# Optimization experiments

Hardware: AMD Instinct MI355X
Metric: run time of the kernel (lower is better)

The kernel has to match this reference:

```python
import jax, jax.numpy as jnp
import numpy as np

B, T, H = 64, 4096, 512


def setup_inputs() -> dict:
    key = jax.random.key(0)
    ks = jax.random.split(key, 6)
    x = jax.random.normal(ks[0], (B, T), dtype=jnp.float32)
    # a ~ U(0.95, 0.999) as in torch init (stable decay)
    a = jax.random.uniform(ks[1], (H,), dtype=jnp.float32, minval=0.95, maxval=0.999)
    b = jax.random.uniform(ks[2], (H,), dtype=jnp.float32, minval=-0.5, maxval=0.5)
    c = jax.random.uniform(ks[3], (H,), dtype=jnp.float32, minval=-0.1, maxval=0.1)
    w = jax.random.uniform(ks[4], (H,), dtype=jnp.float32, minval=-0.5, maxval=0.5)
    e = jax.random.uniform(ks[5], (1,), dtype=jnp.float32, minval=-0.1, maxval=0.1)
    return {"x": x, "a": a, "b": b, "c": c, "w": w, "e": e}


def reference(x, a, b, c, w, e):
    # x: [B, T]; a, b, c, w: [H]; e: [1]
    batch = x.shape[0]
    hidden = a.shape[0]

    def step(h, x_t):
        # h: [B, H]; x_t: [B]
        h = a * h + b * x_t[:, None] + c
        return h, None

    h0 = jnp.zeros((batch, hidden), dtype=x.dtype)
    h, _ = jax.lax.scan(step, h0, x.T)  # scan over T
    z = h @ w + e  # [B]
    return z
```

## Files before the change

### kernel.cpp

```cpp
#include <hip/hip_runtime.h>

#define T_LEN 4096
#define H_LEN 512
#define B_LEN 64

__global__ void build_g_kernel(const float* __restrict__ a,
                               const float* __restrict__ b,
                               const float* __restrict__ c,
                               const float* __restrict__ w,
                               const float* __restrict__ e,
                               float* __restrict__ g,
                               float* __restrict__ Kc)
{
    const int tid = threadIdx.x;
    if (blockIdx.x < T_LEN / 64) {
        __shared__ float wb[H_LEN];
        __shared__ float l2a[H_LEN];
        for (int j = tid; j < H_LEN; j += 256) {
            wb[j]  = w[j] * b[j];
            l2a[j] = log2f(a[j]);
        }
        __syncthreads();
        const int   tt = tid & 63;
        const int   jq = tid >> 6;
        const int   t  = blockIdx.x * 64 + tt;
        const float k  = (float)(T_LEN - 1 - t);
        const int   j0 = jq * (H_LEN / 4);
        float s = 0.f;
#pragma unroll 8
        for (int jj = 0; jj < H_LEN / 4; ++jj) {
            const int j = j0 + jj;
            s += wb[j] * exp2f(k * l2a[j]);
        }
        __shared__ float part[4][64];
        part[jq][tt] = s;
        __syncthreads();
        if (tid < 64) {
            g[blockIdx.x * 64 + tid] =
                part[0][tid] + part[1][tid] + part[2][tid] + part[3][tid];
        }
    } else {
        __shared__ double red[256];
        double s = 0.0;
        for (int j = tid; j < H_LEN; j += 256) {
            const double aj  = (double)a[j];
            const double geo = (1.0 - pow(aj, (double)T_LEN)) / (1.0 - aj);
            s += (double)w[j] * (double)c[j] * geo;
        }
        red[tid] = s;
        __syncthreads();
        for (int off = 128; off > 0; off >>= 1) {
            if (tid < off) red[tid] += red[tid + off];
            __syncthreads();
        }
        if (tid == 0) Kc[0] = (float)(red[0] + (double)e[0]);
    }
}

__global__ void dot_kernel(const float* __restrict__ x,
                           const float* __restrict__ g,
                           const float* __restrict__ Kc,
                           float* __restrict__ z)
{
    const int row = blockIdx.x;
    const int tid = threadIdx.x;
    const float4* __restrict__ xr = (const float4*)(x + (size_t)row * T_LEN);
    const float4* __restrict__ gv = (const float4*)g;
    float s = 0.f;
#pragma unroll
    for (int i = tid; i < T_LEN / 4; i += 256) {
        const float4 xv = xr[i];
        const float4 gg = gv[i];
        s += xv.x * gg.x + xv.y * gg.y + xv.z * gg.z + xv.w * gg.w;
    }
#pragma unroll
    for (int off = 32; off > 0; off >>= 1)
        s += __shfl_down(s, off, 64);
    __shared__ float wsum[4];
    const int wave = tid >> 6;
    if ((tid & 63) == 0) wsum[wave] = s;
    __syncthreads();
    if (tid == 0) {
        z[row] = wsum[0] + wsum[1] + wsum[2] + wsum[3] + Kc[0];
    }
}

extern "C" void kernel_launch(void* const* d_in, const int* in_sizes, int n_in,
                              void* d_out, int out_size, void* d_ws, size_t ws_size,
                              hipStream_t stream) {
    const float* x = (const float*)d_in[0];
    const float* a = (const float*)d_in[1];
    const float* b = (const float*)d_in[2];
    const float* c = (const float*)d_in[3];
    const float* w = (const float*)d_in[4];
    const float* e = (const float*)d_in[5];
    float* out = (float*)d_out;

    float* g  = (float*)d_ws;
    float* Kc = g + T_LEN;

    build_g_kernel<<<T_LEN / 64 + 1, 256, 0, stream>>>(a, b, c, w, e, g, Kc);
    dot_kernel<<<B_LEN, 256, 0, stream>>>(x, g, Kc, out);
}
```

Measured before the change: 68.21 us.

## Fuse weight-kernel build and dot product into one kernel with grid barrier

Merges the two launches into a single kernel. The 64 g-building blocks each also own one batch row of x: they preload it, compute their slice of g, then meet at an atomic counter barrier, waiting on a flag set by the extra Kc block, before doing the dot product. This removes the second launch and the gap between the two kernels, and overlaps the x loads with the exp2 work. In exchange it relies on all blocks being co-resident. The flag is never reset, so on repeated calls a block could increment the counter before the Kc block resets it, which risks a hang.

```diff
diff --git a/kernel.cpp b/kernel.cpp
--- a/kernel.cpp
+++ b/kernel.cpp
@@ -3,43 +3,27 @@
 #define T_LEN 4096
 #define H_LEN 512
 #define B_LEN 64
+#define NGBLK (T_LEN / 64)
 
-__global__ void build_g_kernel(const float* __restrict__ a,
-                               const float* __restrict__ b,
-                               const float* __restrict__ c,
-                               const float* __restrict__ w,
-                               const float* __restrict__ e,
-                               float* __restrict__ g,
-                               float* __restrict__ Kc)
+__global__ __launch_bounds__(256) void fused_kernel(
+    const float* __restrict__ x,
+    const float* __restrict__ a,
+    const float* __restrict__ b,
+    const float* __restrict__ c,
+    const float* __restrict__ w,
+    const float* __restrict__ e,
+    float* __restrict__ g,
+    float* __restrict__ Kc,
+    unsigned int* __restrict__ C,
+    unsigned int* __restrict__ F,
+    float* __restrict__ z)
 {
     const int tid = threadIdx.x;
-    if (blockIdx.x < T_LEN / 64) {
-        __shared__ float wb[H_LEN];
-        __shared__ float l2a[H_LEN];
-        for (int j = tid; j < H_LEN; j += 256) {
-            wb[j]  = w[j] * b[j];
-            l2a[j] = log2f(a[j]);
-        }
-        __syncthreads();
-        const int   tt = tid & 63;
-        const int   jq = tid >> 6;
-        const int   t  = blockIdx.x * 64 + tt;
-        const float k  = (float)(T_LEN - 1 - t);
-        const int   j0 = jq * (H_LEN / 4);
-        float s = 0.f;
-#pragma unroll 8
-        for (int jj = 0; jj < H_LEN / 4; ++jj) {
-            const int j = j0 + jj;
-            s += wb[j] * exp2f(k * l2a[j]);
-        }
-        __shared__ float part[4][64];
-        part[jq][tt] = s;
-        __syncthreads();
-        if (tid < 64) {
-            g[blockIdx.x * 64 + tid] =
-                part[0][tid] + part[1][tid] + part[2][tid] + part[3][tid];
-        }
-    } else {
+    const int blk = blockIdx.x;
+
+    if (blk == NGBLK) {
+        if (tid == 0)
+            __hip_atomic_store(C, 0u, __ATOMIC_RELEASE, __HIP_MEMORY_SCOPE_AGENT);
         __shared__ double red[256];
         double s = 0.0;
         for (int j = tid; j < H_LEN; j += 256) {
@@ -53,36 +37,71 @@
             if (tid < off) red[tid] += red[tid + off];
             __syncthreads();
         }
-        if (tid == 0) Kc[0] = (float)(red[0] + (double)e[0]);
+        if (tid == 0) {
+            Kc[0] = (float)(red[0] + (double)e[0]);
+            __threadfence();
+            __hip_atomic_store(F, 1u, __ATOMIC_RELEASE, __HIP_MEMORY_SCOPE_AGENT);
+        }
+        return;
     }
-}
 
-__global__ void dot_kernel(const float* __restrict__ x,
-                           const float* __restrict__ g,
-                           const float* __restrict__ Kc,
-                           float* __restrict__ z)
-{
-    const int row = blockIdx.x;
-    const int tid = threadIdx.x;
-    const float4* __restrict__ xr = (const float4*)(x + (size_t)row * T_LEN);
+    const float4* __restrict__ xr = (const float4*)(x + (size_t)blk * T_LEN);
+    const float4 xv0 = xr[tid];
+    const float4 xv1 = xr[tid + 256];
+    const float4 xv2 = xr[tid + 512];
+    const float4 xv3 = xr[tid + 768];
+
+    __shared__ float wb[H_LEN];
+    __shared__ float l2a[H_LEN];
+    for (int j = tid; j < H_LEN; j += 256) {
+        wb[j]  = w[j] * b[j];
+        l2a[j] = log2f(a[j]);
+    }
+    __syncthreads();
+    const int   tt = tid & 63;
+    const int   jq = tid >> 6;
+    const int   t  = blk * 64 + tt;
+    const float k  = (float)(T_LEN - 1 - t);
+    const int   j0 = jq * (H_LEN / 4);
+    float s = 0.f;
+#pragma unroll 8
+    for (int jj = 0; jj < H_LEN / 4; ++jj) {
+        const int j = j0 + jj;
+        s += wb[j] * exp2f(k * l2a[j]);
+    }
+    __shared__ float part[4][64];
+    part[jq][tt] = s;
+    __syncthreads();
+    if (tid < 64)
+        g[blk * 64 + tid] = part[0][tid] + part[1][tid] + part[2][tid] + part[3][tid];
+
+    __syncthreads();
+    if (tid == 0) {
+        __threadfence();
+        while (__hip_atomic_load(F, __ATOMIC_ACQUIRE, __HIP_MEMORY_SCOPE_AGENT) != 1u) {}
+        __hip_atomic_fetch_add(C, 1u, __ATOMIC_ACQ_REL, __HIP_MEMORY_SCOPE_AGENT);
+        while (__hip_atomic_load(C, __ATOMIC_ACQUIRE, __HIP_MEMORY_SCOPE_AGENT) != (unsigned)NGBLK) {}
+    }
+    __syncthreads();
+    __threadfence();
+
     const float4* __restrict__ gv = (const float4*)g;
-    float s = 0.f;
-#pragma unroll
-    for (int i = tid; i < T_LEN / 4; i += 256) {
-        const float4 xv = xr[i];
-        const float4 gg = gv[i];
-        s += xv.x * gg.x + xv.y * gg.y + xv.z * gg.z + xv.w * gg.w;
-    }
+    const float4 g0 = gv[tid];
+    const float4 g1 = gv[tid + 256];
+    const float4 g2 = gv[tid + 512];
+    const float4 g3 = gv[tid + 768];
+    float d = xv0.x * g0.x + xv0.y * g0.y + xv0.z * g0.z + xv0.w * g0.w
+            + xv1.x * g1.x + xv1.y * g1.y + xv1.z * g1.z + xv1.w * g1.w
+            + xv2.x * g2.x + xv2.y * g2.y + xv2.z * g2.z + xv2.w * g2.w
+            + xv3.x * g3.x + xv3.y * g3.y + xv3.z * g3.z + xv3.w * g3.w;
 #pragma unroll
     for (int off = 32; off > 0; off >>= 1)
-        s += __shfl_down(s, off, 64);
+        d += __shfl_down(d, off, 64);
     __shared__ float wsum[4];
-    const int wave = tid >> 6;
-    if ((tid & 63) == 0) wsum[wave] = s;
+    if ((tid & 63) == 0) wsum[tid >> 6] = d;
     __syncthreads();
-    if (tid == 0) {
-        z[row] = wsum[0] + wsum[1] + wsum[2] + wsum[3] + Kc[0];
-    }
+    if (tid == 0)
+        z[blk] = wsum[0] + wsum[1] + wsum[2] + wsum[3] + Kc[0];
 }
 
 extern "C" void kernel_launch(void* const* d_in, const int* in_sizes, int n_in,
@@ -96,9 +115,10 @@
     const float* e = (const float*)d_in[5];
     float* out = (float*)d_out;
 
-    float* g  = (float*)d_ws;
-    float* Kc = g + T_LEN;
+    float*        g  = (float*)d_ws;
+    float*        Kc = g + T_LEN;
+    unsigned int* C  = (unsigned int*)(Kc + 1);
+    unsigned int* F  = C + 1;
 
-    build_g_kernel<<<T_LEN / 64 + 1, 256, 0, stream>>>(a, b, c, w, e, g, Kc);
-    dot_kernel<<<B_LEN, 256, 0, stream>>>(x, g, Kc, out);
+    fused_kernel<<<NGBLK + 1, 256, 0, stream>>>(x, a, b, c, w, e, g, Kc, C, F, out);
 }
```

Measured after the change: 74.71 us. 9.5% more time.

## Fuse g-vector construction with per-chunk dot products, reduce partials in finish kernel

Applied to the files above, without the earlier changes.

Each of the 64 time-chunk blocks now builds its slice of the decay-weighted vector g in shared memory and immediately dots it against the matching 64-column slice of x for all 64 rows. It writes per-row, per-chunk partial sums. A single-block finish kernel computes the constant bias term and sums the partials per row. This removes the global round trip for g and spreads the x read across 64 blocks instead of one block per row. The cost is an extra partials buffer and a serial single-block finish stage that also carries the double-precision geometric-sum work.

```diff
diff --git a/kernel.cpp b/kernel.cpp
--- a/kernel.cpp
+++ b/kernel.cpp
@@ -3,85 +3,94 @@
 #define T_LEN 4096
 #define H_LEN 512
 #define B_LEN 64
+#define NCHUNK (T_LEN / 64)
 
-__global__ void build_g_kernel(const float* __restrict__ a,
-                               const float* __restrict__ b,
-                               const float* __restrict__ c,
-                               const float* __restrict__ w,
-                               const float* __restrict__ e,
-                               float* __restrict__ g,
-                               float* __restrict__ Kc)
+__global__ __launch_bounds__(256) void chunk_kernel(
+    const float* __restrict__ x,
+    const float* __restrict__ a,
+    const float* __restrict__ b,
+    const float* __restrict__ w,
+    float* __restrict__ partials)
 {
     const int tid = threadIdx.x;
-    if (blockIdx.x < T_LEN / 64) {
-        __shared__ float wb[H_LEN];
-        __shared__ float l2a[H_LEN];
-        for (int j = tid; j < H_LEN; j += 256) {
-            wb[j]  = w[j] * b[j];
-            l2a[j] = log2f(a[j]);
-        }
-        __syncthreads();
-        const int   tt = tid & 63;
-        const int   jq = tid >> 6;
-        const int   t  = blockIdx.x * 64 + tt;
-        const float k  = (float)(T_LEN - 1 - t);
-        const int   j0 = jq * (H_LEN / 4);
-        float s = 0.f;
+    const int blk = blockIdx.x;
+
+    __shared__ float wb[H_LEN];
+    __shared__ float l2a[H_LEN];
+    for (int j = tid; j < H_LEN; j += 256) {
+        wb[j]  = w[j] * b[j];
+        l2a[j] = log2f(a[j]);
+    }
+    __syncthreads();
+    const int   tt = tid & 63;
+    const int   jq = tid >> 6;
+    const float k  = (float)(T_LEN - 1 - (blk * 64 + tt));
+    const int   j0 = jq * (H_LEN / 4);
+    float s = 0.f;
 #pragma unroll 8
-        for (int jj = 0; jj < H_LEN / 4; ++jj) {
-            const int j = j0 + jj;
-            s += wb[j] * exp2f(k * l2a[j]);
-        }
-        __shared__ float part[4][64];
-        part[jq][tt] = s;
-        __syncthreads();
-        if (tid < 64) {
-            g[blockIdx.x * 64 + tid] =
-                part[0][tid] + part[1][tid] + part[2][tid] + part[3][tid];
-        }
-    } else {
-        __shared__ double red[256];
-        double s = 0.0;
-        for (int j = tid; j < H_LEN; j += 256) {
-            const double aj  = (double)a[j];
-            const double geo = (1.0 - pow(aj, (double)T_LEN)) / (1.0 - aj);
-            s += (double)w[j] * (double)c[j] * geo;
-        }
-        red[tid] = s;
-        __syncthreads();
-        for (int off = 128; off > 0; off >>= 1) {
-            if (tid < off) red[tid] += red[tid + off];
-            __syncthreads();
-        }
-        if (tid == 0) Kc[0] = (float)(red[0] + (double)e[0]);
+    for (int jj = 0; jj < H_LEN / 4; ++jj) {
+        const int j = j0 + jj;
+        s += wb[j] * exp2f(k * l2a[j]);
     }
+    __shared__ float part[4][64];
+    part[jq][tt] = s;
+    __syncthreads();
+    __shared__ float gloc[64];
+    if (tid < 64)
+        gloc[tid] = part[0][tid] + part[1][tid] + part[2][tid] + part[3][tid];
+    __syncthreads();
+
+    const int row = tid >> 2;
+    const int q   = tid & 3;
+    const float4* __restrict__ xp =
+        (const float4*)(x + (size_t)row * T_LEN + blk * 64 + q * 16);
+    const float4* __restrict__ gl = (const float4*)gloc;
+    float d = 0.f;
+#pragma unroll
+    for (int i = 0; i < 4; ++i) {
+        const float4 xv = xp[i];
+        const float4 gv = gl[q * 4 + i];
+        d += xv.x * gv.x + xv.y * gv.y + xv.z * gv.z + xv.w * gv.w;
+    }
+    d += __shfl_xor(d, 1, 64);
+    d += __shfl_xor(d, 2, 64);
+    if (q == 0) partials[row * NCHUNK + blk] = d;
 }
 
-__global__ void dot_kernel(const float* __restrict__ x,
-                           const float* __restrict__ g,
-                           const float* __restrict__ Kc,
-                           float* __restrict__ z)
+__global__ __launch_bounds__(256) void finish_kernel(
+    const float* __restrict__ a,
+    const float* __restrict__ c,
+    const float* __restrict__ w,
+    const float* __restrict__ e,
+    const float* __restrict__ partials,
+    float* __restrict__ z)
 {
-    const int row = blockIdx.x;
     const int tid = threadIdx.x;
-    const float4* __restrict__ xr = (const float4*)(x + (size_t)row * T_LEN);
-    const float4* __restrict__ gv = (const float4*)g;
-    float s = 0.f;
+    __shared__ double red[256];
+    double s = 0.0;
+    for (int j = tid; j < H_LEN; j += 256) {
+        const double aj  = (double)a[j];
+        const double geo = (1.0 - pow(aj, (double)T_LEN)) / (1.0 - aj);
+        s += (double)w[j] * (double)c[j] * geo;
+    }
+    red[tid] = s;
+    __syncthreads();
+    for (int off = 128; off > 0; off >>= 1) {
+        if (tid < off) red[tid] += red[tid + off];
+        __syncthreads();
+    }
+    __shared__ float Ksh;
+    if (tid == 0) Ksh = (float)(red[0] + (double)e[0]);
+    __syncthreads();
+    if (tid < B_LEN) {
+        const float4* __restrict__ pp = (const float4*)(partials + tid * NCHUNK);
+        float acc = 0.f;
 #pragma unroll
-    for (int i = tid; i < T_LEN / 4; i += 256) {
-        const float4 xv = xr[i];
-        const float4 gg = gv[i];
-        s += xv.x * gg.x + xv.y * gg.y + xv.z * gg.z + xv.w * gg.w;
-    }
-#pragma unroll
-    for (int off = 32; off > 0; off >>= 1)
-        s += __shfl_down(s, off, 64);
-    __shared__ float wsum[4];
-    const int wave = tid >> 6;
-    if ((tid & 63) == 0) wsum[wave] = s;
-    __syncthreads();
-    if (tid == 0) {
-        z[row] = wsum[0] + wsum[1] + wsum[2] + wsum[3] + Kc[0];
+        for (int i = 0; i < NCHUNK / 4; ++i) {
+            const float4 v = pp[i];
+            acc += v.x + v.y + v.z + v.w;
+        }
+        z[tid] = acc + Ksh;
     }
 }
 
@@ -96,9 +105,8 @@
     const float* e = (const float*)d_in[5];
     float* out = (float*)d_out;
 
-    float* g  = (float*)d_ws;
-    float* Kc = g + T_LEN;
+    float* partials = (float*)d_ws;
 
-    build_g_kernel<<<T_LEN / 64 + 1, 256, 0, stream>>>(a, b, c, w, e, g, Kc);
-    dot_kernel<<<B_LEN, 256, 0, stream>>>(x, g, Kc, out);
+    chunk_kernel<<<NCHUNK, 256, 0, stream>>>(x, a, b, w, partials);
+    finish_kernel<<<1, 256, 0, stream>>>(a, c, w, e, partials, out);
 }
```

Result: slower. 70.70 us (+3.7%).
